# Kernel optimization log

Hardware: AMD Instinct MI355X
Metric: run time of the kernel (lower is better)

The kernel has to match this reference:

```python
import jax, jax.numpy as jnp
import numpy as np
from functools import partial

INPUT_DIM = 256
HIDDEN = 512
NUM_LAYERS = 2

def _linp(key, fan_in, shape):
    # torch nn.Linear/Conv default init: U(-1/sqrt(fan_in), 1/sqrt(fan_in))
    bound = 1.0 / np.sqrt(fan_in)
    return jax.random.uniform(key, shape, jnp.float32, -bound, bound)

def setup_inputs() -> dict:
    key = jax.random.key(0)
    ks = iter(jax.random.split(key, 64))
    d = {}
    d["x"] = jax.random.normal(next(ks), (32, 16, 1, 64, 64), jnp.float32)
    # encoder convs (OIHW)
    d["conv1_w"] = _linp(next(ks), 1 * 9, (16, 1, 3, 3));   d["conv1_b"] = _linp(next(ks), 1 * 9, (16,))
    d["conv2_w"] = _linp(next(ks), 16 * 9, (32, 16, 3, 3)); d["conv2_b"] = _linp(next(ks), 16 * 9, (32,))
    d["conv3_w"] = _linp(next(ks), 32 * 9, (INPUT_DIM, 32, 3, 3)); d["conv3_b"] = _linp(next(ks), 32 * 9, (INPUT_DIM,))
    # LSTM cells: per layer 4 gate linears (forget, input, cell, output), in = input+hidden
    for j in range(NUM_LAYERS):
        fan = (INPUT_DIM if j == 0 else HIDDEN) + HIDDEN
        for g in ("f", "i", "g", "o"):
            d[f"W{g}{j}"] = _linp(next(ks), fan, (fan, HIDDEN))
            d[f"b{g}{j}"] = _linp(next(ks), fan, (HIDDEN,))
    # classifier
    d["cw1"] = _linp(next(ks), HIDDEN, (HIDDEN, 128)); d["cb1"] = _linp(next(ks), HIDDEN, (128,))
    d["cw2"] = _linp(next(ks), 128, (128, 64));        d["cb2"] = _linp(next(ks), 128, (64,))
    d["cw3"] = _linp(next(ks), 64, (64, 6));           d["cb3"] = _linp(next(ks), 64, (6,))
    return d

def _conv(x, w, b):
    y = jax.lax.conv_general_dilated(x, w, (1, 1), "SAME",
                                     dimension_numbers=("NCHW", "OIHW", "NCHW"))
    return y + b[None, :, None, None]

def _maxpool2(x):
    return jax.lax.reduce_window(x, -jnp.inf, jax.lax.max,
                                 (1, 1, 2, 2), (1, 1, 2, 2), "VALID")

def reference(x, conv1_w, conv1_b, conv2_w, conv2_b, conv3_w, conv3_b,
              Wf0, bf0, Wi0, bi0, Wg0, bg0, Wo0, bo0,
              Wf1, bf1, Wi1, bi1, Wg1, bg1, Wo1, bo1,
              cw1, cb1, cw2, cb2, cw3, cb3):
    B, T, C, H, W = x.shape
    xf = x.reshape(B * T, C, H, W)
    h = _maxpool2(jax.nn.relu(_conv(xf, conv1_w, conv1_b)))
    h = _maxpool2(jax.nn.relu(_conv(h, conv2_w, conv2_b)))
    h = jax.nn.relu(_conv(h, conv3_w, conv3_b))
    emb = h.mean(axis=(2, 3)).reshape(B, T, -1)  # AdaptiveAvgPool2d((1,1)); dropout = identity (eval)

    layers = [(Wf0, bf0, Wi0, bi0, Wg0, bg0, Wo0, bo0),
              (Wf1, bf1, Wi1, bi1, Wg1, bg1, Wo1, bo1)]

    def step(carry, x_t):
        hs, cs = carry
        inp = x_t
        new_h, new_c = [], []
        for j, (Wf, bf, Wi, bi, Wg, bg, Wo, bo) in enumerate(layers):
            comb = jnp.concatenate([inp, hs[j]], axis=1)  # [B, in+H]
            f_t = jax.nn.sigmoid(comb @ Wf + bf)
            i_t = jax.nn.sigmoid(comb @ Wi + bi)
            g_t = jnp.tanh(comb @ Wg + bg)
            o_t = jax.nn.sigmoid(comb @ Wo + bo)
            c_n = f_t * cs[j] + i_t * g_t
            h_n = o_t * jnp.tanh(c_n)
            new_h.append(h_n); new_c.append(c_n)
            inp = h_n
        return (tuple(new_h), tuple(new_c)), None

    h0 = tuple(jnp.zeros((B, HIDDEN), x.dtype) for _ in range(NUM_LAYERS))
    c0 = tuple(jnp.zeros((B, HIDDEN), x.dtype) for _ in range(NUM_LAYERS))
    (hs, _), _ = jax.lax.scan(step, (h0, c0), jnp.swapaxes(emb, 0, 1))
    last = hs[-1]  # [B, HIDDEN], last timestep top-layer h (dropout = identity)

    y = jax.nn.relu(last @ cw1 + cb1)
    y = jax.nn.relu(y @ cw2 + cb2)
    return y @ cw3 + cb3  # [B, 6]
```

## Files before the change

kernel.cpp:

```cpp
#include <hip/hip_runtime.h>
#include <math.h>

__global__ void k_conv1(const float* __restrict__ x, const float* __restrict__ w,
                        const float* __restrict__ bias, float* __restrict__ out) {
  int idx = blockIdx.x * 256 + threadIdx.x;
  int ox = idx & 31, oy = (idx >> 5) & 31, oc = (idx >> 10) & 15, n = idx >> 14;
  const float* im = x + n * 4096;
  float wv[9];
#pragma unroll
  for (int i = 0; i < 9; ++i) wv[i] = w[oc * 9 + i];
  float bs = bias[oc];
  float m = 0.f;
#pragma unroll
  for (int dy = 0; dy < 2; ++dy)
#pragma unroll
    for (int dx = 0; dx < 2; ++dx) {
      int cy = oy * 2 + dy, cx = ox * 2 + dx;
      float s = bs;
#pragma unroll
      for (int ky = 0; ky < 3; ++ky) {
        int yy = cy + ky - 1;
        if (yy < 0 || yy >= 64) continue;
#pragma unroll
        for (int kx = 0; kx < 3; ++kx) {
          int xx = cx + kx - 1;
          if (xx < 0 || xx >= 64) continue;
          s += im[yy * 64 + xx] * wv[ky * 3 + kx];
        }
      }
      m = fmaxf(m, fmaxf(s, 0.f));
    }
  out[idx] = m;
}

__global__ void k_prep_w(const float* __restrict__ w2, float* __restrict__ w2t,
                         const float* __restrict__ w3, float* __restrict__ w3t) {
  int id = blockIdx.x * 256 + threadIdx.x;
  if (id < 73728) {
    int ct = id >> 8, oc = id & 255;
    int c = ct / 9, tap = ct - 9 * c;
    w3t[id] = w3[(oc * 32 + c) * 9 + tap];
  }
  if (id < 4608) {
    int ct = id >> 5, oc = id & 31;
    int c = ct / 9, tap = ct - 9 * c;
    w2t[id] = w2[(oc * 16 + c) * 9 + tap];
  }
}

__global__ __launch_bounds__(256) void k_conv2(
    const float* __restrict__ a1, const float* __restrict__ w2t,
    const float* __restrict__ bias, float* __restrict__ a2) {
  __shared__ __align__(16) float ins[8 * 1024];
  int n = blockIdx.x, ocg = blockIdx.y;
  int tid = threadIdx.x;
  int py = tid >> 4, px = tid & 15;
  int y0 = 2 * py - 1, x0 = 2 * px - 1;
  float acc[16][4] = {};
  const float* wb = w2t + ocg * 16;
  for (int ph = 0; ph < 2; ++ph) {
    __syncthreads();
    const float4* src = (const float4*)(a1 + n * 16384 + ph * 8192);
    for (int i = tid; i < 2048; i += 256) ((float4*)ins)[i] = src[i];
    __syncthreads();
    for (int c = 0; c < 8; ++c) {
      float wv[4][4];
#pragma unroll
      for (int r = 0; r < 4; ++r) {
        int y = y0 + r;
        bool vy = (y >= 0) && (y < 32);
        int yc = vy ? y : 0;
#pragma unroll
        for (int cc = 0; cc < 4; ++cc) {
          int xx = x0 + cc;
          bool vx = (xx >= 0) && (xx < 32);
          int xc = vx ? xx : 0;
          float t = ins[c * 1024 + yc * 32 + xc];
          wv[r][cc] = (vy && vx) ? t : 0.f;
        }
      }
      int ch = ph * 8 + c;
#pragma unroll
      for (int ky = 0; ky < 3; ++ky)
#pragma unroll
        for (int kx = 0; kx < 3; ++kx) {
          const float* w16 = wb + (ch * 9 + ky * 3 + kx) * 32;
#pragma unroll
          for (int i = 0; i < 4; ++i) {
            float vv = wv[(i >> 1) + ky][(i & 1) + kx];
#pragma unroll
            for (int j = 0; j < 16; ++j) acc[j][i] += vv * w16[j];
          }
        }
    }
  }
  const float* bp = bias + ocg * 16;
  float4 o[4];
#pragma unroll
  for (int j = 0; j < 16; ++j) {
    float m = fmaxf(fmaxf(acc[j][0], acc[j][1]), fmaxf(acc[j][2], acc[j][3]));
    ((float*)o)[j] = fmaxf(m + bp[j], 0.f);
  }
  float4* dst = (float4*)(a2 + (size_t)(n * 256 + tid) * 32 + ocg * 16);
#pragma unroll
  for (int q = 0; q < 4; ++q) dst[q] = o[q];
}

__global__ __launch_bounds__(256) void k_conv3(
    const float* __restrict__ a2, const float* __restrict__ w3t,
    const float* __restrict__ bias, float* __restrict__ comb0) {
  __shared__ __align__(16) float ins[324 * 20];
  int n = blockIdx.x, ocb = blockIdx.y;
  int tid = threadIdx.x;
  for (int i = tid; i < 1620; i += 256) ((float4*)ins)[i] = float4{0.f, 0.f, 0.f, 0.f};
  int wvid = __builtin_amdgcn_readfirstlane(tid >> 6);
  int lane = tid & 63;
  int tr = lane >> 4, tc = lane & 15;
  float acc[4][8] = {};
  const float* wbase = w3t + ocb * 32 + wvid * 8;
  const float4* src = (const float4*)(a2 + (size_t)n * 8192);
  for (int hf = 0; hf < 2; ++hf) {
    __syncthreads();
    for (int i = tid; i < 1024; i += 256) {
      int px = i >> 2, cg = i & 3;
      int p = ((px >> 4) + 1) * 18 + (px & 15) + 1;
      ((float4*)ins)[p * 5 + cg] = src[px * 8 + hf * 4 + cg];
    }
    __syncthreads();
    for (int cg = 0; cg < 4; ++cg) {
      float4 v[6][3];
#pragma unroll
      for (int dr = 0; dr < 6; ++dr)
#pragma unroll
        for (int dc = 0; dc < 3; ++dc)
          v[dr][dc] = ((const float4*)ins)[((4 * tr + dr) * 18 + tc + dc) * 5 + cg];
#pragma unroll
      for (int ky = 0; ky < 3; ++ky)
#pragma unroll
        for (int kx = 0; kx < 3; ++kx)
#pragma unroll
          for (int c = 0; c < 4; ++c) {
            const float* w8 = wbase + (((hf * 4 + cg) * 4 + c) * 9 + ky * 3 + kx) * 256;
#pragma unroll
            for (int i = 0; i < 4; ++i) {
              float vv = ((const float*)&v[i + ky][kx])[c];
#pragma unroll
              for (int j = 0; j < 8; ++j) acc[i][j] += vv * w8[j];
            }
          }
    }
  }
  const float* bp = bias + ocb * 32 + wvid * 8;
  int bb = n >> 4, tt = n & 15;
#pragma unroll
  for (int j = 0; j < 8; ++j) {
    float bj = bp[j];
    float s = 0.f;
#pragma unroll
    for (int i = 0; i < 4; ++i) s += fmaxf(acc[i][j] + bj, 0.f);
#pragma unroll
    for (int off = 32; off; off >>= 1) s += __shfl_down(s, off, 64);
    if (lane == 0) {
      int oc = ocb * 32 + wvid * 8 + j;
      comb0[(size_t)(tt * 768 + oc) * 32 + bb] = s * (1.f / 256.f);
    }
  }
}

__global__ void k_pack(const float* __restrict__ Wf, const float* __restrict__ Wi,
                       const float* __restrict__ Wg, const float* __restrict__ Wo,
                       float* __restrict__ p, int fan) {
  __shared__ float t[4][32][33];
  int k0 = blockIdx.x * 32, h0 = blockIdx.y * 32;
  int tx = threadIdx.x & 31, ty = threadIdx.x >> 5;
  const float* Ws[4] = {Wf, Wi, Wg, Wo};
#pragma unroll
  for (int g = 0; g < 4; ++g)
    for (int r = 0; r < 32; r += 8)
      t[g][ty + r][tx] = Ws[g][(size_t)(k0 + ty + r) * 512 + h0 + tx];
  __syncthreads();
  for (int r = 0; r < 32; r += 8) {
    int hh = ty + r;
    float4 v = {t[0][tx][hh], t[1][tx][hh], t[2][tx][hh], t[3][tx][hh]};
    ((float4*)p)[(size_t)(h0 + hh) * fan + k0 + tx] = v;
  }
}

struct Coop2Args {
  float* comb0; float* comb1;
  const float* p0; const float* p1;
  const float* b00; const float* b01; const float* b02; const float* b03;
  const float* b10; const float* b11; const float* b12; const float* b13;
  int* bar;
};

#define COOP2_LDS_BYTES (31744 * 4)

template <bool DO0, bool DO1>
__device__ __forceinline__ void fused_step(
    int hbase, int tid, int it, const Coop2Args& A,
    const float4* __restrict__ w40, const float4* __restrict__ w41,
    float* __restrict__ gsum0, float* __restrict__ gsum1,
    float* __restrict__ pre,
    float bf, float bi, float bg, float bo, float& creg) {
  const int C0 = 768 * 32, C1 = 1024 * 32;
  const int hs = tid >> 8, kc = (tid >> 3) & 31, bq = tid & 7;
  const int rot = kc & 7;
  float4 f0{0,0,0,0}, i0{0,0,0,0}, g0{0,0,0,0}, o0{0,0,0,0};
  float4 f1{0,0,0,0}, i1{0,0,0,0}, g1{0,0,0,0}, o1{0,0,0,0};
  if constexpr (DO1) {
    const float4* a41 = (const float4*)(A.comb1 + (size_t)(it - 1) * C1);
#pragma unroll
    for (int kk = 0; kk < 32; ++kk) {
      int idx = kk + rot; if (idx >= 32) idx -= 32;
      float4 w = w41[idx];
      float4 a = a41[(size_t)(kc * 32 + idx) * 8 + bq];
      f1.x += w.x*a.x; f1.y += w.x*a.y; f1.z += w.x*a.z; f1.w += w.x*a.w;
      i1.x += w.y*a.x; i1.y += w.y*a.y; i1.z += w.y*a.z; i1.w += w.y*a.w;
      g1.x += w.z*a.x; g1.y += w.z*a.y; g1.z += w.z*a.z; g1.w += w.z*a.w;
      o1.x += w.w*a.x; o1.y += w.w*a.y; o1.z += w.w*a.z; o1.w += w.w*a.w;
    }
  }
  if constexpr (DO0) {
    const float4* a40 = (const float4*)(A.comb0 + (size_t)it * C0);
#pragma unroll
    for (int kk = 0; kk < 24; ++kk) {
      int idx = kk + rot; if (idx >= 24) idx -= 24;
      float4 w = w40[idx];
      float4 a = a40[(size_t)(kc * 24 + idx) * 8 + bq];
      f0.x += w.x*a.x; f0.y += w.x*a.y; f0.z += w.x*a.z; f0.w += w.x*a.w;
      i0.x += w.y*a.x; i0.y += w.y*a.y; i0.z += w.y*a.z; i0.w += w.y*a.w;
      g0.x += w.z*a.x; g0.y += w.z*a.y; g0.z += w.z*a.z; g0.w += w.z*a.w;
      o0.x += w.w*a.x; o0.y += w.w*a.y; o0.z += w.w*a.z; o0.w += w.w*a.w;
    }
  }
  __syncthreads();
  if constexpr (DO0) {
    const float* accs[4] = {(const float*)&f0, (const float*)&i0,
                            (const float*)&g0, (const float*)&o0};
#pragma unroll
    for (int g = 0; g < 4; ++g)
#pragma unroll
      for (int j = 0; j < 4; ++j)
        gsum0[((hs * 4 + g) * 32 + 4 * bq + j) * 33 + kc] = accs[g][j];
  }
  if constexpr (DO1) {
    const float* accs[4] = {(const float*)&f1, (const float*)&i1,
                            (const float*)&g1, (const float*)&o1};
#pragma unroll
    for (int g = 0; g < 4; ++g)
#pragma unroll
      for (int j = 0; j < 4; ++j)
        gsum1[((hs * 4 + g) * 32 + 4 * bq + j) * 33 + kc] = accs[g][j];
  }
  __syncthreads();
  {
    int l = tid >> 8, idx = tid & 255;
    int hs2 = idx >> 7, g = (idx >> 5) & 3, b = idx & 31;
    if ((DO0 && l == 0) || (DO1 && l == 1)) {
      const float* gs = l ? gsum1 : gsum0;
      int base = ((hs2 * 4 + g) * 32 + b) * 33;
      float s = 0.f;
#pragma unroll
      for (int q = 0; q < 32; ++q) s += gs[base + q];
      pre[l * 256 + (hs2 * 4 + g) * 32 + b] = s;
    }
  }
  __syncthreads();
  if (tid < 128) {
    int l = tid >> 6, hs2 = (tid >> 5) & 1, b = tid & 31;
    if ((DO0 && l == 0) || (DO1 && l == 1)) {
      const float* pr = pre + l * 256;
      float fp = pr[(hs2 * 4 + 0) * 32 + b] + bf;
      float ip = pr[(hs2 * 4 + 1) * 32 + b] + bi;
      float gp = pr[(hs2 * 4 + 2) * 32 + b] + bg;
      float op = pr[(hs2 * 4 + 3) * 32 + b] + bo;
      float ft = 1.f / (1.f + expf(-fp));
      float it_ = 1.f / (1.f + expf(-ip));
      float gt = tanhf(gp);
      float ot = 1.f / (1.f + expf(-op));
      float cn = ft * creg + it_ * gt;
      creg = cn;
      float hn = ot * tanhf(cn);
      int hh = hbase + hs2;
      if (l == 0) {
        float* hA = A.comb0 + (size_t)(it + 1) * C0 + 256 * 32;
        float* hB = A.comb1 + (size_t)it * C1;
        __hip_atomic_store(&hA[hh * 32 + b], hn, __ATOMIC_RELAXED,
                           __HIP_MEMORY_SCOPE_AGENT);
        __hip_atomic_store(&hB[hh * 32 + b], hn, __ATOMIC_RELAXED,
                           __HIP_MEMORY_SCOPE_AGENT);
      } else {
        float* hA = A.comb1 + (size_t)it * C1 + 512 * 32;
        __hip_atomic_store(&hA[hh * 32 + b], hn, __ATOMIC_RELAXED,
                           __HIP_MEMORY_SCOPE_AGENT);
      }
    }
  }
}

__device__ __forceinline__ void coop_barrier(int* bar, int tid, int it) {
  __syncthreads();
  if (tid == 0) {
    __hip_atomic_fetch_add(bar, 1, __ATOMIC_RELEASE, __HIP_MEMORY_SCOPE_AGENT);
    const int target = 256 * (it + 1);
    while (__hip_atomic_load(bar, __ATOMIC_RELAXED,
                             __HIP_MEMORY_SCOPE_AGENT) < target)
      __builtin_amdgcn_s_sleep(8);
    __builtin_amdgcn_fence(__ATOMIC_ACQUIRE, "agent");
  }
  __syncthreads();
}

__global__ __launch_bounds__(512) void k_lstm_coop2(Coop2Args A) {
  extern __shared__ float smem[];
  float* wl0 = smem;
  float* wl1 = smem + 6144;
  float* gsum0 = smem + 14336;
  float* gsum1 = smem + 22784;
  float* pre = smem + 31232;
  const int tid = threadIdx.x;
  const int hbase = blockIdx.x * 2;
  for (int i = tid; i < 1536; i += 512) {
    int hs = (i >= 768), k = i - hs * 768;
    ((float4*)wl0)[hs * 768 + k] =
        ((const float4*)A.p0)[(size_t)(hbase + hs) * 768 + k];
  }
  for (int i = tid; i < 2048; i += 512) {
    int hs = i >> 10, k = i & 1023;
    ((float4*)wl1)[hs * 1024 + k] =
        ((const float4*)A.p1)[(size_t)(hbase + hs) * 1024 + k];
  }
  float bf = 0, bi = 0, bg = 0, bo = 0, creg = 0.f;
  if (tid < 64) {
    int hh = hbase + (tid >> 5);
    bf = A.b00[hh]; bi = A.b01[hh]; bg = A.b02[hh]; bo = A.b03[hh];
  } else if (tid < 128) {
    int hh = hbase + ((tid >> 5) & 1);
    bf = A.b10[hh]; bi = A.b11[hh]; bg = A.b12[hh]; bo = A.b13[hh];
  }
  __syncthreads();
  const int hs = tid >> 8, kc = (tid >> 3) & 31;
  const float4* w40 = (const float4*)wl0 + (size_t)hs * 768 + kc * 24;
  const float4* w41 = (const float4*)wl1 + (size_t)hs * 1024 + kc * 32;

  fused_step<true, false>(hbase, tid, 0, A, w40, w41, gsum0, gsum1, pre,
                          bf, bi, bg, bo, creg);
  coop_barrier(A.bar, tid, 0);
  for (int it = 1; it < 16; ++it) {
    fused_step<true, true>(hbase, tid, it, A, w40, w41, gsum0, gsum1, pre,
                           bf, bi, bg, bo, creg);
    coop_barrier(A.bar, tid, it);
  }
  fused_step<false, true>(hbase, tid, 16, A, w40, w41, gsum0, gsum1, pre,
                          bf, bi, bg, bo, creg);
}

struct SArgs {
  const float* comb; const float* pw;
  float* houtA; float* houtB; float* cT;
  const float* bf; const float* bi; const float* bg; const float* bo;
};

template <int FAN>
__device__ __forceinline__ void lstm_sbody(int h, int tid, const SArgs& A,
                                           float* __restrict__ gsum) {
  constexpr int CH = FAN / 8;
  const int wv = __builtin_amdgcn_readfirstlane(tid >> 6);
  const int lane = tid & 63;
  const int ks = lane >> 5, b = lane & 31;
  const int kb = wv * CH;
  const float4* pw4 = (const float4*)A.pw + (size_t)h * FAN + kb;
  const float* ac = A.comb + (size_t)kb * 32 + lane;
  float a0 = 0.f, a1 = 0.f, a2 = 0.f, a3 = 0.f;
#pragma unroll 8
  for (int kk = 0; kk < CH; kk += 2) {
    float4 w0 = pw4[kk];
    float4 w1 = pw4[kk + 1];
    float av = ac[kk * 32];
    a0 += av * (ks ? w1.x : w0.x);
    a1 += av * (ks ? w1.y : w0.y);
    a2 += av * (ks ? w1.z : w0.z);
    a3 += av * (ks ? w1.w : w0.w);
  }
  a0 += __shfl_xor(a0, 32);
  a1 += __shfl_xor(a1, 32);
  a2 += __shfl_xor(a2, 32);
  a3 += __shfl_xor(a3, 32);
  if (lane < 32) {
    gsum[(wv * 4 + 0) * 33 + b] = a0;
    gsum[(wv * 4 + 1) * 33 + b] = a1;
    gsum[(wv * 4 + 2) * 33 + b] = a2;
    gsum[(wv * 4 + 3) * 33 + b] = a3;
  }
  __syncthreads();
  if (tid < 32) {
    float fp = A.bf[h], ip = A.bi[h], gp = A.bg[h], op = A.bo[h];
#pragma unroll
    for (int q = 0; q < 8; ++q) {
      fp += gsum[(q * 4 + 0) * 33 + tid];
      ip += gsum[(q * 4 + 1) * 33 + tid];
      gp += gsum[(q * 4 + 2) * 33 + tid];
      op += gsum[(q * 4 + 3) * 33 + tid];
    }
    float ft = 1.f / (1.f + expf(-fp));
    float it_ = 1.f / (1.f + expf(-ip));
    float gt = tanhf(gp);
    float ot = 1.f / (1.f + expf(-op));
    float cn = ft * A.cT[h * 32 + tid] + it_ * gt;
    A.cT[h * 32 + tid] = cn;
    float hn = ot * tanhf(cn);
    A.houtA[h * 32 + tid] = hn;
    A.houtB[h * 32 + tid] = hn;
  }
}

__global__ __launch_bounds__(512) void k_lstm_s0(SArgs a) {
  __shared__ float gsum[32 * 33];
  lstm_sbody<768>(blockIdx.x, threadIdx.x, a, gsum);
}
__global__ __launch_bounds__(512) void k_lstm_s1(SArgs a) {
  __shared__ float gsum[32 * 33];
  lstm_sbody<1024>(blockIdx.x, threadIdx.x, a, gsum);
}
__global__ __launch_bounds__(512) void k_lstm_spair(SArgs a0, SArgs a1) {
  __shared__ float gsum[32 * 33];
  if (blockIdx.x < 512)
    lstm_sbody<768>(blockIdx.x, threadIdx.x, a0, gsum);
  else
    lstm_sbody<1024>(blockIdx.x - 512, threadIdx.x, a1, gsum);
}

__global__ void k_cls(const float* __restrict__ h1T, const float* __restrict__ cw1,
                      const float* __restrict__ cb1, const float* __restrict__ cw2,
                      const float* __restrict__ cb2, const float* __restrict__ cw3,
                      const float* __restrict__ cb3, float* __restrict__ out) {
  __shared__ float hv[512];
  __shared__ float y1[128];
  __shared__ float y2[64];
  int b = blockIdx.x, tid = threadIdx.x;
  for (int i = tid; i < 512; i += 128) hv[i] = h1T[i * 32 + b];
  __syncthreads();
  float s = cb1[tid];
  for (int k = 0; k < 512; ++k) s += hv[k] * cw1[k * 128 + tid];
  y1[tid] = fmaxf(s, 0.f);
  __syncthreads();
  if (tid < 64) {
    float s2 = cb2[tid];
    for (int k = 0; k < 128; ++k) s2 += y1[k] * cw2[k * 64 + tid];
    y2[tid] = fmaxf(s2, 0.f);
  }
  __syncthreads();
  if (tid < 6) {
    float s3 = cb3[tid];
    for (int k = 0; k < 64; ++k) s3 += y2[k] * cw3[k * 6 + tid];
    out[b * 6 + tid] = s3;
  }
}

extern "C" void kernel_launch(void* const* d_in, const int* in_sizes, int n_in,
                              void* d_out, int out_size, void* d_ws, size_t ws_size,
                              hipStream_t stream) {
  const float* x  = (const float*)d_in[0];
  const float* w1 = (const float*)d_in[1];
  const float* b1 = (const float*)d_in[2];
  const float* w2 = (const float*)d_in[3];
  const float* b2 = (const float*)d_in[4];
  const float* w3 = (const float*)d_in[5];
  const float* b3 = (const float*)d_in[6];
  const float* cw1 = (const float*)d_in[23];
  const float* cb1 = (const float*)d_in[24];
  const float* cw2 = (const float*)d_in[25];
  const float* cb2 = (const float*)d_in[26];
  const float* cw3 = (const float*)d_in[27];
  const float* cb3 = (const float*)d_in[28];

  float* ws = (float*)d_ws;
  float* a1    = ws;
  float* p0    = ws;
  float* p1    = ws + 1572864;
  float* comb0 = ws + 3670016;
  float* comb1 = ws + 4087808;
  float* c0    = ws + 4644864;
  float* c1    = ws + 4661248;
  int*   bar   = (int*)(ws + 4677632);
  float* a2    = ws + 8388608;
  float* w2t   = ws + 12582912;
  float* w3t   = ws + 12587520;
  const int C0 = 768 * 32, C1 = 1024 * 32;

  k_prep_w<<<288, 256, 0, stream>>>(w2, w2t, w3, w3t);
  k_conv1<<<32768, 256, 0, stream>>>(x, w1, b1, a1);
  k_conv2<<<dim3(512, 2), 256, 0, stream>>>(a1, w2t, b2, a2);

  hipMemsetAsync(comb0 + 256 * 32, 0, (size_t)512 * 32 * 4, stream);
  hipMemsetAsync(comb1 + 512 * 32, 0, (size_t)512 * 32 * 4, stream);
  hipMemsetAsync(c0, 0, (size_t)2 * 512 * 32 * 4, stream);
  hipMemsetAsync(bar, 0, sizeof(int), stream);

  k_conv3<<<dim3(512, 8), 256, 0, stream>>>(a2, w3t, b3, comb0);

  k_pack<<<dim3(24, 16), 256, 0, stream>>>(
      (const float*)d_in[7], (const float*)d_in[9],
      (const float*)d_in[11], (const float*)d_in[13], p0, 768);
  k_pack<<<dim3(32, 16), 256, 0, stream>>>(
      (const float*)d_in[15], (const float*)d_in[17],
      (const float*)d_in[19], (const float*)d_in[21], p1, 1024);

  Coop2Args ca;
  ca.comb0 = comb0; ca.comb1 = comb1;
  ca.p0 = p0; ca.p1 = p1;
  ca.b00 = (const float*)d_in[8];  ca.b01 = (const float*)d_in[10];
  ca.b02 = (const float*)d_in[12]; ca.b03 = (const float*)d_in[14];
  ca.b10 = (const float*)d_in[16]; ca.b11 = (const float*)d_in[18];
  ca.b12 = (const float*)d_in[20]; ca.b13 = (const float*)d_in[22];
  ca.bar = bar;
  void* kargs[] = {&ca};
  hipError_t cerr = hipLaunchCooperativeKernel(
      (void*)k_lstm_coop2, dim3(256), dim3(512), kargs, COOP2_LDS_BYTES, stream);

  if (cerr != hipSuccess) {
    auto L0 = [&](int t) {
      SArgs a;
      a.comb = comb0 + (size_t)t * C0;
      a.pw = p0;
      a.houtA = comb0 + (size_t)(t + 1) * C0 + 256 * 32;
      a.houtB = comb1 + (size_t)t * C1;
      a.cT = c0;
      a.bf = (const float*)d_in[8];  a.bi = (const float*)d_in[10];
      a.bg = (const float*)d_in[12]; a.bo = (const float*)d_in[14];
      return a;
    };
    auto L1 = [&](int t) {
      SArgs a;
      a.comb = comb1 + (size_t)t * C1;
      a.pw = p1;
      a.houtA = comb1 + (size_t)(t + 1) * C1 + 512 * 32;
      a.houtB = a.houtA;
      a.cT = c1;
      a.bf = (const float*)d_in[16]; a.bi = (const float*)d_in[18];
      a.bg = (const float*)d_in[20]; a.bo = (const float*)d_in[22];
      return a;
    };
    k_lstm_s0<<<512, 512, 0, stream>>>(L0(0));
    for (int p = 0; p < 15; ++p)
      k_lstm_spair<<<1024, 512, 0, stream>>>(L0(p + 1), L1(p));
    k_lstm_s1<<<512, 512, 0, stream>>>(L1(15));
  }

  k_cls<<<32, 128, 0, stream>>>(comb1 + (size_t)16 * C1 + 512 * 32,
                                cw1, cb1, cw2, cb2, cw3, cb3, (float*)d_out);
}
```

Baseline: 618.5 us.

## Use hierarchical grid barrier and strided K-interleaving in LSTM coop kernel

```diff
diff --git a/kernel.cpp b/kernel.cpp
--- a/kernel.cpp
+++ b/kernel.cpp
@@ -205,16 +205,15 @@
     float bf, float bi, float bg, float bo, float& creg) {
   const int C0 = 768 * 32, C1 = 1024 * 32;
   const int hs = tid >> 8, kc = (tid >> 3) & 31, bq = tid & 7;
-  const int rot = kc & 7;
   float4 f0{0,0,0,0}, i0{0,0,0,0}, g0{0,0,0,0}, o0{0,0,0,0};
   float4 f1{0,0,0,0}, i1{0,0,0,0}, g1{0,0,0,0}, o1{0,0,0,0};
   if constexpr (DO1) {
-    const float4* a41 = (const float4*)(A.comb1 + (size_t)(it - 1) * C1);
+    const float4* a41 = (const float4*)(A.comb1 + (size_t)(it - 1) * C1)
+                        + kc * 8 + bq;
 #pragma unroll
     for (int kk = 0; kk < 32; ++kk) {
-      int idx = kk + rot; if (idx >= 32) idx -= 32;
-      float4 w = w41[idx];
-      float4 a = a41[(size_t)(kc * 32 + idx) * 8 + bq];
+      float4 w = w41[kk * 32];
+      float4 a = a41[kk * 256];
       f1.x += w.x*a.x; f1.y += w.x*a.y; f1.z += w.x*a.z; f1.w += w.x*a.w;
       i1.x += w.y*a.x; i1.y += w.y*a.y; i1.z += w.y*a.z; i1.w += w.y*a.w;
       g1.x += w.z*a.x; g1.y += w.z*a.y; g1.z += w.z*a.z; g1.w += w.z*a.w;
@@ -222,12 +221,12 @@
     }
   }
   if constexpr (DO0) {
-    const float4* a40 = (const float4*)(A.comb0 + (size_t)it * C0);
+    const float4* a40 = (const float4*)(A.comb0 + (size_t)it * C0)
+                        + kc * 8 + bq;
 #pragma unroll
     for (int kk = 0; kk < 24; ++kk) {
-      int idx = kk + rot; if (idx >= 24) idx -= 24;
-      float4 w = w40[idx];
-      float4 a = a40[(size_t)(kc * 24 + idx) * 8 + bq];
+      float4 w = w40[kk * 32];
+      float4 a = a40[kk * 256];
       f0.x += w.x*a.x; f0.y += w.x*a.y; f0.z += w.x*a.z; f0.w += w.x*a.w;
       i0.x += w.y*a.x; i0.y += w.y*a.y; i0.z += w.y*a.z; i0.w += w.y*a.w;
       g0.x += w.z*a.x; g0.y += w.z*a.y; g0.z += w.z*a.z; g0.w += w.z*a.w;
@@ -299,14 +298,19 @@
   }
 }
 
-__device__ __forceinline__ void coop_barrier(int* bar, int tid, int it) {
+__device__ __forceinline__ void coop_barrier(int* bars, int tid, int bid,
+                                             int it) {
   __syncthreads();
   if (tid == 0) {
-    __hip_atomic_fetch_add(bar, 1, __ATOMIC_RELEASE, __HIP_MEMORY_SCOPE_AGENT);
-    const int target = 256 * (it + 1);
-    while (__hip_atomic_load(bar, __ATOMIC_RELAXED,
-                             __HIP_MEMORY_SCOPE_AGENT) < target)
-      __builtin_amdgcn_s_sleep(8);
+    int* gb = bars + 32 + (bid & 7) * 32;
+    int old = __hip_atomic_fetch_add(gb, 1, __ATOMIC_ACQ_REL,
+                                     __HIP_MEMORY_SCOPE_AGENT);
+    if (old == 32 * (it + 1) - 1)
+      __hip_atomic_fetch_add(bars, 1, __ATOMIC_RELEASE,
+                             __HIP_MEMORY_SCOPE_AGENT);
+    while (__hip_atomic_load(bars, __ATOMIC_RELAXED,
+                             __HIP_MEMORY_SCOPE_AGENT) < 8 * (it + 1))
+      __builtin_amdgcn_s_sleep(2);
     __builtin_amdgcn_fence(__ATOMIC_ACQUIRE, "agent");
   }
   __syncthreads();
@@ -341,16 +345,16 @@
   }
   __syncthreads();
   const int hs = tid >> 8, kc = (tid >> 3) & 31;
-  const float4* w40 = (const float4*)wl0 + (size_t)hs * 768 + kc * 24;
-  const float4* w41 = (const float4*)wl1 + (size_t)hs * 1024 + kc * 32;
+  const float4* w40 = (const float4*)wl0 + (size_t)hs * 768 + kc;
+  const float4* w41 = (const float4*)wl1 + (size_t)hs * 1024 + kc;
 
   fused_step<true, false>(hbase, tid, 0, A, w40, w41, gsum0, gsum1, pre,
                           bf, bi, bg, bo, creg);
-  coop_barrier(A.bar, tid, 0);
+  coop_barrier(A.bar, tid, blockIdx.x, 0);
   for (int it = 1; it < 16; ++it) {
     fused_step<true, true>(hbase, tid, it, A, w40, w41, gsum0, gsum1, pre,
                            bf, bi, bg, bo, creg);
-    coop_barrier(A.bar, tid, it);
+    coop_barrier(A.bar, tid, blockIdx.x, it);
   }
   fused_step<false, true>(hbase, tid, 16, A, w40, w41, gsum0, gsum1, pre,
                           bf, bi, bg, bo, creg);
@@ -496,7 +500,7 @@
   hipMemsetAsync(comb0 + 256 * 32, 0, (size_t)512 * 32 * 4, stream);
   hipMemsetAsync(comb1 + 512 * 32, 0, (size_t)512 * 32 * 4, stream);
   hipMemsetAsync(c0, 0, (size_t)2 * 512 * 32 * 4, stream);
-  hipMemsetAsync(bar, 0, sizeof(int), stream);
+  hipMemsetAsync(bar, 0, 512 * sizeof(int), stream);
 
   k_conv3<<<dim3(512, 8), 256, 0, stream>>>(a2, w3t, b3, comb0);
 
```

Measured after the change: 612.0 us. Within noise of the previous version (-1.0%).
